# Performance work log

Hardware: AMD Instinct MI355X
Metric: run time of the kernel (lower is better)

The kernel has to match this reference:

```python
import jax, jax.numpy as jnp
import numpy as np


def setup_inputs() -> dict:
    key = jax.random.key(0)
    ks = jax.random.split(key, 7)
    B, C, H, W = 32, 512, 64, 64
    C8 = C // 8
    scale = 1.0 / np.sqrt(C)  # ~kaiming-ish for 1x1 conv
    return {
        "x": jax.random.normal(ks[0], (B, C, H, W), dtype=jnp.float32),
        "wq": jax.random.normal(ks[1], (C8, C), dtype=jnp.float32) * scale,
        "bq": jax.random.normal(ks[2], (C8,), dtype=jnp.float32) * 0.01,
        "wk": jax.random.normal(ks[3], (C8, C), dtype=jnp.float32) * scale,
        "bk": jax.random.normal(ks[4], (C8,), dtype=jnp.float32) * 0.01,
        "wv": jax.random.normal(ks[5], (C8, C), dtype=jnp.float32) * scale,
        "bv": jax.random.normal(ks[6], (C8,), dtype=jnp.float32) * 0.01,
    }


def reference(x, wq, bq, wk, bk, wv, bv):
    B, C, H, W = x.shape
    N = H * W
    xf = x.reshape(B, C, N)  # [B, C, N]
    # 1x1 convs == per-pixel linear projections C -> C//8
    q = jnp.einsum("bcn,oc->bon", xf, wq) + bq[None, :, None]  # [B, C8, N]
    k = jnp.einsum("bcn,oc->bon", xf, wk) + bk[None, :, None]  # [B, C8, N]
    v = jnp.einsum("bcn,oc->bon", xf, wv) + bv[None, :, None]  # [B, C8, N]
    # attention over channel pairs: [B, C8, C8], softmax over dim=-2 (rows)
    logits = jnp.einsum("bon,bpn->bop", q, k)
    attn = jax.nn.softmax(logits, axis=-2)
    out = jnp.einsum("bop,bpn->bon", attn, v)  # [B, C8, N]
    return out.mean(axis=-1)  # [B, C8]
```

## Files before the change

### kernel.cpp

```cpp
#include <hip/hip_runtime.h>


typedef __attribute__((ext_vector_type(8))) short short8;
typedef __attribute__((ext_vector_type(4))) float floatx4;
typedef __attribute__((ext_vector_type(4))) unsigned short ushort4v;
typedef __attribute__((ext_vector_type(8))) unsigned short ushort8v;

#define MFMA16(a, b, c) __builtin_amdgcn_mfma_f32_16x16x32_bf16((a), (b), (c), 0, 0, 0)

__device__ __forceinline__ unsigned short f2bf(float f) {
  unsigned int u = __float_as_uint(f);
  u = u + 0x7fffu + ((u >> 16) & 1u);
  return (unsigned short)(u >> 16);
}
__device__ __forceinline__ float bf2f(unsigned short h) {
  return __uint_as_float(((unsigned int)h) << 16);
}

constexpr int CB = 32;
constexpr int CC = 512;
constexpr int CO = 64;
constexpr int NN = 4096;
constexpr int NT = 128;
constexpr int KC = 32;
constexpr int NCH = CC / KC;

constexpr int XROW = 40;
constexpr int QROW = 72;

constexpr int WQH = 0;
constexpr int WQL = 2560;
constexpr int WKH = 5120;
constexpr int WKL = 7680;
constexpr int XHI = 10240;
constexpr int XLO = 15360;
constexpr int SMEM_U = 20480;
constexpr int QHI = 0, QLO = 4608, KHI = 9216, KLO = 13824;

constexpr int WB_ELEMS = CO * CC;

__global__ __launch_bounds__(256) void prep_kernel(
    const float* __restrict__ wq, const float* __restrict__ wk,
    unsigned short* __restrict__ wbuf)
{
  const int i = blockIdx.x * 256 + threadIdx.x;
  const float q = wq[i], k = wk[i];
  const unsigned short qh = f2bf(q), kh = f2bf(k);
  wbuf[i]                 = qh;
  wbuf[WB_ELEMS + i]      = f2bf(q - bf2f(qh));
  wbuf[2 * WB_ELEMS + i]  = kh;
  wbuf[3 * WB_ELEMS + i]  = f2bf(k - bf2f(kh));
}

__global__ __launch_bounds__(256, 2) void proj_kernel(
    const float* __restrict__ x, const unsigned short* __restrict__ wbuf,
    const float* __restrict__ bq, const float* __restrict__ bk,
    float* __restrict__ logits, float* __restrict__ xsum)
{
  __shared__ __align__(16) unsigned short smem[SMEM_U];

  const int t    = threadIdx.x;
  const int lane = t & 63;
  const int wave = t >> 6;
  const int quad = lane >> 4;
  const int l15  = lane & 15;
  const int b    = blockIdx.x >> 5;
  const int tile = blockIdx.x & 31;
  const int n0   = tile * NT;
  const int nlow = t & 31;
  const int chi  = t >> 5;
  const int wrow = t >> 2;
  const int wcf  = (t & 3) * 8;

  floatx4 accq[4][2], acck[4][2];
#pragma unroll
  for (int mf = 0; mf < 4; ++mf)
#pragma unroll
    for (int nf = 0; nf < 2; ++nf) {
      accq[mf][nf] = (floatx4)0.0f;
      acck[mf][nf] = (floatx4)0.0f;
    }

  const float* xb = x + (size_t)b * CC * NN + n0;

  float xr[16];
#pragma unroll
  for (int i = 0; i < 4; ++i)
#pragma unroll
    for (int cj = 0; cj < 4; ++cj)
      xr[i * 4 + cj] = xb[(size_t)(chi * 4 + cj) * NN + i * 32 + nlow];

  for (int ch = 0; ch < NCH; ++ch) {
    const int c0 = ch * KC;
    __syncthreads();

    const unsigned short* wsrc = wbuf + (size_t)wrow * CC + c0 + wcf;
    const ushort8v a0 = *reinterpret_cast<const ushort8v*>(wsrc);
    const ushort8v a1 = *reinterpret_cast<const ushort8v*>(wsrc + WB_ELEMS);
    const ushort8v a2 = *reinterpret_cast<const ushort8v*>(wsrc + 2 * WB_ELEMS);
    const ushort8v a3 = *reinterpret_cast<const ushort8v*>(wsrc + 3 * WB_ELEMS);

    float xs_part[4] = {0.f, 0.f, 0.f, 0.f};
#pragma unroll
    for (int i = 0; i < 4; ++i) {
      const int n = i * 32 + nlow;
      const float v0 = xr[i * 4 + 0], v1 = xr[i * 4 + 1];
      const float v2 = xr[i * 4 + 2], v3 = xr[i * 4 + 3];
      xs_part[0] += v0; xs_part[1] += v1; xs_part[2] += v2; xs_part[3] += v3;
      ushort4v h, l;
      h[0] = f2bf(v0); l[0] = f2bf(v0 - bf2f(h[0]));
      h[1] = f2bf(v1); l[1] = f2bf(v1 - bf2f(h[1]));
      h[2] = f2bf(v2); l[2] = f2bf(v2 - bf2f(h[2]));
      h[3] = f2bf(v3); l[3] = f2bf(v3 - bf2f(h[3]));
      *reinterpret_cast<ushort4v*>(&smem[XHI + n * XROW + chi * 4]) = h;
      *reinterpret_cast<ushort4v*>(&smem[XLO + n * XROW + chi * 4]) = l;
    }
#pragma unroll
    for (int j = 0; j < 4; ++j) {
      float v = xs_part[j];
      v += __shfl_xor(v, 16); v += __shfl_xor(v, 8);
      v += __shfl_xor(v, 4);  v += __shfl_xor(v, 2); v += __shfl_xor(v, 1);
      if ((lane & 31) == 0) atomicAdd(&xsum[b * CC + c0 + chi * 4 + j], v);
    }

    *reinterpret_cast<ushort8v*>(&smem[WQH + wrow * XROW + wcf]) = a0;
    *reinterpret_cast<ushort8v*>(&smem[WQL + wrow * XROW + wcf]) = a1;
    *reinterpret_cast<ushort8v*>(&smem[WKH + wrow * XROW + wcf]) = a2;
    *reinterpret_cast<ushort8v*>(&smem[WKL + wrow * XROW + wcf]) = a3;

    if (ch + 1 < NCH) {
      const int c0n = c0 + KC;
#pragma unroll
      for (int i = 0; i < 4; ++i)
#pragma unroll
        for (int cj = 0; cj < 4; ++cj)
          xr[i * 4 + cj] = xb[(size_t)(c0n + chi * 4 + cj) * NN + i * 32 + nlow];
    }
    __syncthreads();

    short8 xh[2], xl[2];
#pragma unroll
    for (int nf = 0; nf < 2; ++nf) {
      const int nr = wave * 32 + nf * 16 + l15;
      xh[nf] = *reinterpret_cast<const short8*>(&smem[XHI + nr * XROW + quad * 8]);
      xl[nf] = *reinterpret_cast<const short8*>(&smem[XLO + nr * XROW + quad * 8]);
    }
#pragma unroll
    for (int mf = 0; mf < 4; ++mf) {
      const int orow = mf * 16 + l15;
      const short8 aqh = *reinterpret_cast<const short8*>(&smem[WQH + orow * XROW + quad * 8]);
      const short8 aql = *reinterpret_cast<const short8*>(&smem[WQL + orow * XROW + quad * 8]);
      const short8 akh = *reinterpret_cast<const short8*>(&smem[WKH + orow * XROW + quad * 8]);
      const short8 akl = *reinterpret_cast<const short8*>(&smem[WKL + orow * XROW + quad * 8]);
#pragma unroll
      for (int nf = 0; nf < 2; ++nf) {
        accq[mf][nf] = MFMA16(aqh, xh[nf], accq[mf][nf]);
        accq[mf][nf] = MFMA16(aql, xh[nf], accq[mf][nf]);
        accq[mf][nf] = MFMA16(aqh, xl[nf], accq[mf][nf]);
        acck[mf][nf] = MFMA16(akh, xh[nf], acck[mf][nf]);
        acck[mf][nf] = MFMA16(akl, xh[nf], acck[mf][nf]);
        acck[mf][nf] = MFMA16(akh, xl[nf], acck[mf][nf]);
      }
    }
  }

#pragma unroll
  for (int mf = 0; mf < 4; ++mf)
#pragma unroll
    for (int r = 0; r < 4; ++r) {
      const int o = mf * 16 + quad * 4 + r;
      const float bqv = bq[o], bkv = bk[o];
#pragma unroll
      for (int nf = 0; nf < 2; ++nf) {
        accq[mf][nf][r] += bqv;
        acck[mf][nf][r] += bkv;
      }
    }

  floatx4 accS[4];
#pragma unroll
  for (int mf = 0; mf < 4; ++mf) accS[mf] = (floatx4)0.0f;

  for (int hh = 0; hh < 2; ++hh) {
    __syncthreads();
    if ((wave >> 1) == hh) {
      const int nbase = (wave & 1) * 32;
#pragma unroll
      for (int mf = 0; mf < 4; ++mf)
#pragma unroll
        for (int nf = 0; nf < 2; ++nf)
#pragma unroll
          for (int r = 0; r < 4; ++r) {
            const int o  = mf * 16 + quad * 4 + r;
            const int nc = nbase + nf * 16 + l15;
            const float qv = accq[mf][nf][r];
            const float kv = acck[mf][nf][r];
            const unsigned short qh = f2bf(qv);
            const unsigned short kh = f2bf(kv);
            smem[QHI + o * QROW + nc] = qh;
            smem[QLO + o * QROW + nc] = f2bf(qv - bf2f(qh));
            smem[KHI + o * QROW + nc] = kh;
            smem[KLO + o * QROW + nc] = f2bf(kv - bf2f(kh));
          }
    }
    __syncthreads();
#pragma unroll
    for (int ks = 0; ks < 2; ++ks) {
      const short8 bh = *reinterpret_cast<const short8*>(
          &smem[KHI + (wave * 16 + l15) * QROW + ks * 32 + quad * 8]);
      const short8 bl = *reinterpret_cast<const short8*>(
          &smem[KLO + (wave * 16 + l15) * QROW + ks * 32 + quad * 8]);
#pragma unroll
      for (int mf = 0; mf < 4; ++mf) {
        const short8 ah = *reinterpret_cast<const short8*>(
            &smem[QHI + (mf * 16 + l15) * QROW + ks * 32 + quad * 8]);
        const short8 al = *reinterpret_cast<const short8*>(
            &smem[QLO + (mf * 16 + l15) * QROW + ks * 32 + quad * 8]);
        accS[mf] = MFMA16(ah, bh, accS[mf]);
        accS[mf] = MFMA16(al, bh, accS[mf]);
        accS[mf] = MFMA16(ah, bl, accS[mf]);
      }
    }
  }

#pragma unroll
  for (int mf = 0; mf < 4; ++mf)
#pragma unroll
    for (int r = 0; r < 4; ++r) {
      const int o = mf * 16 + quad * 4 + r;
      const int p = wave * 16 + l15;
      atomicAdd(&logits[((size_t)b * CO + o) * CO + p], accS[mf][r]);
    }
}

__global__ __launch_bounds__(256) void zero_kernel(float* __restrict__ p, int n) {
  const int i = blockIdx.x * 256 + threadIdx.x;
  if (i < n) p[i] = 0.0f;
}

__global__ __launch_bounds__(256) void finalize_kernel(
    const float* __restrict__ wv, const float* __restrict__ bv,
    const float* __restrict__ logits, const float* __restrict__ xsum,
    float* __restrict__ out)
{
  __shared__ float ls[CO * 65];
  __shared__ float xs_s[CC];
  __shared__ float vbar_s[CO], w2_s[CO], cmax_s[CO];
  const int t = threadIdx.x;
  const int b = blockIdx.x;

  for (int i = t; i < CC; i += 256) xs_s[i] = xsum[b * CC + i];
#pragma unroll
  for (int i = 0; i < 16; ++i) {
    const int idx = t + i * 256;
    ls[(idx >> 6) * 65 + (idx & 63)] = logits[(size_t)b * CO * CO + idx];
  }
  __syncthreads();

  {
    const int p = t >> 2, part = t & 3;
    float s = 0.f;
    const float* wr = wv + (size_t)p * CC + part * 128;
    const float* xr = xs_s + part * 128;
#pragma unroll 4
    for (int c = 0; c < 128; ++c) s += wr[c] * xr[c];
    s += __shfl_xor(s, 1); s += __shfl_xor(s, 2);
    if (part == 0) vbar_s[p] = s * (1.0f / 4096.0f) + bv[p];
  }
  __syncthreads();

  if (t < CO) {
    float m = -1e30f;
    for (int o = 0; o < CO; ++o) m = fmaxf(m, ls[o * 65 + t]);
    float sum = 0.f;
    for (int o = 0; o < CO; ++o) sum += __expf(ls[o * 65 + t] - m);
    cmax_s[t] = m;
    w2_s[t]   = vbar_s[t] / sum;
  }
  __syncthreads();

  if (t < CO) {
    float acc = 0.f;
    for (int p = 0; p < CO; ++p)
      acc += __expf(ls[t * 65 + p] - cmax_s[p]) * w2_s[p];
    out[b * CO + t] = acc;
  }
}

extern "C" void kernel_launch(void* const* d_in, const int* in_sizes, int n_in,
                              void* d_out, int out_size, void* d_ws, size_t ws_size,
                              hipStream_t stream) {
  const float* x  = (const float*)d_in[0];
  const float* wq = (const float*)d_in[1];
  const float* bq = (const float*)d_in[2];
  const float* wk = (const float*)d_in[3];
  const float* bk = (const float*)d_in[4];
  const float* wv = (const float*)d_in[5];
  const float* bv = (const float*)d_in[6];
  float* out = (float*)d_out;

  float* logits = (float*)d_ws;
  float* xsum   = logits + CB * CO * CO;
  const int nzero = CB * CO * CO + CB * CC;
  unsigned short* wbuf = (unsigned short*)(xsum + CB * CC);

  zero_kernel<<<(nzero + 255) / 256, 256, 0, stream>>>(logits, nzero);
  prep_kernel<<<WB_ELEMS / 256, 256, 0, stream>>>(wq, wk, wbuf);
  proj_kernel<<<CB * (NN / NT), 256, 0, stream>>>(x, wbuf, bq, bk, logits, xsum);
  finalize_kernel<<<CB, 256, 0, stream>>>(wv, bv, wbuf ? logits : logits, xsum, out);
}
```

Before: 398.8 us.

## Double-buffer x register prefetch two chunks ahead and merge init kernels

The projection loop now keeps two register buffers of x and issues the global loads for chunk ch+2 while processing chunk ch. This gives the loads more time in flight before they are needed. The two __syncthreads calls are replaced by an explicit LDS waitcnt plus s_barrier, and the weight LDS stores are moved earlier. The zero and weight-prep kernels are fused into one launch to save a kernel dispatch. The extra 16-float buffer raises register pressure under the existing launch bounds of 256 threads with 2 blocks per unit.

```diff
diff --git a/kernel.cpp b/kernel.cpp
--- a/kernel.cpp
+++ b/kernel.cpp
@@ -15,6 +15,11 @@
 }
 __device__ __forceinline__ float bf2f(unsigned short h) {
   return __uint_as_float(((unsigned int)h) << 16);
+}
+
+__device__ __forceinline__ void barrier_lds() {
+  asm volatile("s_waitcnt lgkmcnt(0)" ::: "memory");
+  __builtin_amdgcn_s_barrier();
 }
 
 constexpr int CB = 32;
@@ -38,18 +43,22 @@
 constexpr int QHI = 0, QLO = 4608, KHI = 9216, KLO = 13824;
 
 constexpr int WB_ELEMS = CO * CC;
-
-__global__ __launch_bounds__(256) void prep_kernel(
+constexpr int ZERO_N = CB * CO * CO + CB * CC;
+
+__global__ __launch_bounds__(256) void init_kernel(
     const float* __restrict__ wq, const float* __restrict__ wk,
-    unsigned short* __restrict__ wbuf)
+    unsigned short* __restrict__ wbuf, float* __restrict__ zp)
 {
   const int i = blockIdx.x * 256 + threadIdx.x;
-  const float q = wq[i], k = wk[i];
-  const unsigned short qh = f2bf(q), kh = f2bf(k);
-  wbuf[i]                 = qh;
-  wbuf[WB_ELEMS + i]      = f2bf(q - bf2f(qh));
-  wbuf[2 * WB_ELEMS + i]  = kh;
-  wbuf[3 * WB_ELEMS + i]  = f2bf(k - bf2f(kh));
+  if (i < ZERO_N) zp[i] = 0.0f;
+  if (i < WB_ELEMS) {
+    const float q = wq[i], k = wk[i];
+    const unsigned short qh = f2bf(q), kh = f2bf(k);
+    wbuf[i]                 = qh;
+    wbuf[WB_ELEMS + i]      = f2bf(q - bf2f(qh));
+    wbuf[2 * WB_ELEMS + i]  = kh;
+    wbuf[3 * WB_ELEMS + i]  = f2bf(k - bf2f(kh));
+  }
 }
 
 __global__ __launch_bounds__(256, 2) void proj_kernel(
@@ -83,16 +92,18 @@
 
   const float* xb = x + (size_t)b * CC * NN + n0;
 
-  float xr[16];
-#pragma unroll
-  for (int i = 0; i < 4; ++i)
-#pragma unroll
-    for (int cj = 0; cj < 4; ++cj)
-      xr[i * 4 + cj] = xb[(size_t)(chi * 4 + cj) * NN + i * 32 + nlow];
-
-  for (int ch = 0; ch < NCH; ++ch) {
+  auto loadx = [&](float (&xr)[16], int ch) {
     const int c0 = ch * KC;
-    __syncthreads();
+#pragma unroll
+    for (int i = 0; i < 4; ++i)
+#pragma unroll
+      for (int cj = 0; cj < 4; ++cj)
+        xr[i * 4 + cj] = xb[(size_t)(c0 + chi * 4 + cj) * NN + i * 32 + nlow];
+  };
+
+  auto body = [&](int ch, float (&xr)[16]) {
+    const int c0 = ch * KC;
+    barrier_lds();
 
     const unsigned short* wsrc = wbuf + (size_t)wrow * CC + c0 + wcf;
     const ushort8v a0 = *reinterpret_cast<const ushort8v*>(wsrc);
@@ -115,6 +126,14 @@
       *reinterpret_cast<ushort4v*>(&smem[XHI + n * XROW + chi * 4]) = h;
       *reinterpret_cast<ushort4v*>(&smem[XLO + n * XROW + chi * 4]) = l;
     }
+
+    if (ch + 2 < NCH) loadx(xr, ch + 2);
+
+    *reinterpret_cast<ushort8v*>(&smem[WQH + wrow * XROW + wcf]) = a0;
+    *reinterpret_cast<ushort8v*>(&smem[WQL + wrow * XROW + wcf]) = a1;
+    *reinterpret_cast<ushort8v*>(&smem[WKH + wrow * XROW + wcf]) = a2;
+    *reinterpret_cast<ushort8v*>(&smem[WKL + wrow * XROW + wcf]) = a3;
+
 #pragma unroll
     for (int j = 0; j < 4; ++j) {
       float v = xs_part[j];
@@ -122,21 +141,7 @@
       v += __shfl_xor(v, 4);  v += __shfl_xor(v, 2); v += __shfl_xor(v, 1);
       if ((lane & 31) == 0) atomicAdd(&xsum[b * CC + c0 + chi * 4 + j], v);
     }
-
-    *reinterpret_cast<ushort8v*>(&smem[WQH + wrow * XROW + wcf]) = a0;
-    *reinterpret_cast<ushort8v*>(&smem[WQL + wrow * XROW + wcf]) = a1;
-    *reinterpret_cast<ushort8v*>(&smem[WKH + wrow * XROW + wcf]) = a2;
-    *reinterpret_cast<ushort8v*>(&smem[WKL + wrow * XROW + wcf]) = a3;
-
-    if (ch + 1 < NCH) {
-      const int c0n = c0 + KC;
-#pragma unroll
-      for (int i = 0; i < 4; ++i)
-#pragma unroll
-        for (int cj = 0; cj < 4; ++cj)
-          xr[i * 4 + cj] = xb[(size_t)(c0n + chi * 4 + cj) * NN + i * 32 + nlow];
-    }
-    __syncthreads();
+    barrier_lds();
 
     short8 xh[2], xl[2];
 #pragma unroll
@@ -162,6 +167,15 @@
         acck[mf][nf] = MFMA16(akh, xl[nf], acck[mf][nf]);
       }
     }
+  };
+
+  float xr0[16], xr1[16];
+  loadx(xr0, 0);
+  loadx(xr1, 1);
+#pragma unroll 1
+  for (int ch = 0; ch < NCH; ch += 2) {
+    body(ch, xr0);
+    body(ch + 1, xr1);
   }
 
 #pragma unroll
@@ -233,11 +247,6 @@
     }
 }
 
-__global__ __launch_bounds__(256) void zero_kernel(float* __restrict__ p, int n) {
-  const int i = blockIdx.x * 256 + threadIdx.x;
-  if (i < n) p[i] = 0.0f;
-}
-
 __global__ __launch_bounds__(256) void finalize_kernel(
     const float* __restrict__ wv, const float* __restrict__ bv,
     const float* __restrict__ logits, const float* __restrict__ xsum,
@@ -301,11 +310,9 @@
 
   float* logits = (float*)d_ws;
   float* xsum   = logits + CB * CO * CO;
-  const int nzero = CB * CO * CO + CB * CC;
   unsigned short* wbuf = (unsigned short*)(xsum + CB * CC);
 
-  zero_kernel<<<(nzero + 255) / 256, 256, 0, stream>>>(logits, nzero);
-  prep_kernel<<<WB_ELEMS / 256, 256, 0, stream>>>(wq, wk, wbuf);
+  init_kernel<<<(ZERO_N + 255) / 256, 256, 0, stream>>>(wq, wk, wbuf, logits);
   proj_kernel<<<CB * (NN / NT), 256, 0, stream>>>(x, wbuf, bq, bk, logits, xsum);
-  finalize_kernel<<<CB, 256, 0, stream>>>(wv, bv, wbuf ? logits : logits, xsum, out);
-}
+  finalize_kernel<<<CB, 256, 0, stream>>>(wv, bv, logits, xsum, out);
+}
```

Result: no change. 406.4 us (+1.9%).
